# Kernel tuning notes

Measured on AMD Instinct MI355X. Metric: run time of the kernel, lower is better.

Reference implementation:

```python
import jax, jax.numpy as jnp
import numpy as np

B = 16384      # rays
H = 128        # field hidden dim


def setup_inputs() -> dict:
    key = jax.random.key(0)
    ks = jax.random.split(key, 8)
    origins = jax.random.normal(ks[0], (B, 3), dtype=jnp.float32)
    directions = jax.random.normal(ks[1], (B, 3), dtype=jnp.float32)
    directions = directions / jnp.linalg.norm(directions, axis=-1, keepdims=True)
    # Field: simple MLP 3 -> H -> H -> 4 (rgb + sigma)
    W1 = jax.random.normal(ks[2], (3, H), dtype=jnp.float32) * (1.0 / np.sqrt(3.0))
    b1 = jnp.zeros((H,), dtype=jnp.float32)
    W2 = jax.random.normal(ks[3], (H, H), dtype=jnp.float32) * (1.0 / np.sqrt(H))
    b2 = jnp.zeros((H,), dtype=jnp.float32)
    W3 = jax.random.normal(ks[4], (H, 4), dtype=jnp.float32) * (1.0 / np.sqrt(H))
    b3 = jnp.zeros((4,), dtype=jnp.float32)
    return {"origins": origins, "directions": directions,
            "W1": W1, "b1": b1, "W2": W2, "b2": b2, "W3": W3, "b3": b3,
            "near": 2, "far": 6, "num_samples": 64}


def _field(x, W1, b1, W2, b2, W3, b3):
    h = jax.nn.relu(x @ W1 + b1)
    h = jax.nn.relu(h @ W2 + b2)
    return h @ W3 + b3


def reference(origins, directions, W1, b1, W2, b2, W3, b3, near, far, num_samples):
    near = jnp.float32(near)
    far = jnp.float32(far)
    # 1. generate_samples: segment boundaries + midpoints along each ray
    depths = jnp.linspace(near, far, num_samples + 1)            # [S+1]
    midpoints = 0.5 * (depths[:-1] + depths[1:])                 # [S]
    # [B, S, 3] = origin + t * direction
    locs = origins[:, None, :] + midpoints[None, :, None] * directions[:, None, :]
    # 2. evaluate field
    f = _field(locs.reshape(-1, 3), W1, b1, W2, b2, W3, b3)
    f = f.reshape(origins.shape[0], num_samples, 4)
    # NOTE: source overwrites the sigmoid'd colors with raw outputs (faithful)
    colors = f[..., :3]                                          # [B, S, 3]
    sigma = f[..., 3]                                            # [B, S]
    # 3. alpha values
    delta = depths[1:] - depths[:-1]                             # [S]
    alphas = 1.0 - jnp.exp(-sigma * delta[None, :])              # [B, S]
    # 4. alpha compositing (black background)
    ones = jnp.ones_like(alphas[:, :1])
    transmittance = jnp.cumprod(jnp.concatenate([ones, 1.0 - alphas], axis=1), axis=1)[:, :-1]
    weights = alphas * transmittance                             # [B, S]
    radiance = jnp.sum(weights[..., None] * colors, axis=1)      # [B, 3]
    return radiance
```

## Files before the change

### kernel.cpp

```cpp
#include <hip/hip_runtime.h>


typedef _Float16 f16;
typedef __attribute__((ext_vector_type(2))) _Float16 h2v;
typedef __attribute__((ext_vector_type(8))) _Float16 half8;
typedef __attribute__((ext_vector_type(4))) float floatx4;

#define H 128
#define NS 64

static __device__ __forceinline__ h2v pkrtz(float a, float b) {
  return __builtin_bit_cast(h2v, __builtin_amdgcn_cvt_pkrtz(a, b));
}

template <int CTRL, int RM>
static __device__ __forceinline__ float dpp_add(float x) {
  int sh = __builtin_amdgcn_update_dpp(0, __builtin_bit_cast(int, x),
                                       CTRL, RM, 0xf, false);
  return x + __builtin_bit_cast(float, sh);
}

static __device__ __forceinline__ float wave_iscan(float x) {
  x = dpp_add<0x111, 0xf>(x);
  x = dpp_add<0x112, 0xf>(x);
  x = dpp_add<0x114, 0xf>(x);
  x = dpp_add<0x118, 0xf>(x);
  x = dpp_add<0x142, 0xa>(x);
  x = dpp_add<0x143, 0xc>(x);
  return x;
}

__global__ void nerf_setup(const float* __restrict__ W2, const float* __restrict__ W3,
                           f16* __restrict__ wsW2, f16* __restrict__ wsW3) {
  int t = blockIdx.x * blockDim.x + threadIdx.x;
  if (t < 8192) {
    int j2 = t & 3, lane = (t >> 2) & 63, mt = (t >> 8) & 7, ks = t >> 11;
    int l16 = lane & 15;
    int k = ks * 32 + ((lane >> 4) * 8) + 2 * j2;
    int n = 32 * (l16 >> 2) + mt * 4 + (l16 & 3);
    wsW2[2 * t]     = (f16)W2[k * H + n];
    wsW2[2 * t + 1] = (f16)W2[(k + 1) * H + n];
  } else if (t < 9216) {
    int u = t - 8192;
    int j2 = u & 3, lane = (u >> 2) & 63, ks = u >> 8;
    int c = lane & 15;
    int k3 = 32 * (lane >> 4) + ks * 8 + 2 * j2;
    wsW3[2 * u]     = (c < 4) ? (f16)W3[k3 * 4 + c]       : (f16)0.0f;
    wsW3[2 * u + 1] = (c < 4) ? (f16)W3[(k3 + 1) * 4 + c] : (f16)0.0f;
  }
}

__global__ __launch_bounds__(512, 4) void nerf_main(
    const float* __restrict__ origins, const float* __restrict__ dirs,
    const float* __restrict__ W1, const float* __restrict__ b1,
    const float* __restrict__ b2, const float* __restrict__ b3,
    const f16* __restrict__ ws,
    float* __restrict__ out)
{
  __shared__ __align__(16) half8 w_lds[2304];
  __shared__ __align__(16) float b2_lds[H];
  __shared__ __align__(16) f16   popd[8][2][H];
  __shared__ __align__(16) float f_lds[8][64][4];

  const int t = threadIdx.x;
  const int w = t >> 6, lane = t & 63, quad = lane >> 4, l16 = lane & 15;
  const float delta = 4.0f / NS;
  const int ray = blockIdx.x * 8 + w;

  {
    const uint4* src = (const uint4*)ws;
    uint4* dst = (uint4*)w_lds;
    #pragma unroll
    for (int i = 0; i < 4; ++i) dst[t + i * 512] = src[t + i * 512];
    if (t < 256) dst[t + 2048] = src[t + 2048];
    if (t < 32)  ((float4*)b2_lds)[t] = ((const float4*)b2)[t];
  }

  {
    const float o0 = origins[ray*3], o1 = origins[ray*3+1], o2 = origins[ray*3+2];
    const float d0 = dirs[ray*3],    d1 = dirs[ray*3+1],    d2 = dirs[ray*3+2];
    const int k0 = lane * 2;
    const float2 wr0 = *(const float2*)&W1[0*H + k0];
    const float2 wr1 = *(const float2*)&W1[1*H + k0];
    const float2 wr2 = *(const float2*)&W1[2*H + k0];
    const float2 bb  = *(const float2*)&b1[k0];
    float poa = fmaf(o2, wr2.x, fmaf(o1, wr1.x, fmaf(o0, wr0.x, bb.x)));
    float pob = fmaf(o2, wr2.y, fmaf(o1, wr1.y, fmaf(o0, wr0.y, bb.y)));
    float pda = fmaf(d2, wr2.x, fmaf(d1, wr1.x, d0 * wr0.x));
    float pdb = fmaf(d2, wr2.y, fmaf(d1, wr1.y, d0 * wr0.y));
    h2v po2; po2[0] = (f16)poa; po2[1] = (f16)pob;
    h2v pd2; pd2[0] = (f16)pda; pd2[1] = (f16)pdb;
    *(h2v*)&popd[w][0][k0] = po2;
    *(h2v*)&popd[w][1][k0] = pd2;
  }

  half8 hb[4][4];
  {
    const half8 z8 = (half8)(f16)0.0f;
    half8 m8[4];
    #pragma unroll
    for (int tr = 0; tr < 4; ++tr)
      m8[tr] = (half8)(f16)(2.0f + (tr*16 + l16 + 0.5f) * delta);
    #pragma unroll
    for (int ks = 0; ks < 4; ++ks) {
      const half8 po8 = *(const half8*)&popd[w][0][ks*32 + quad*8];
      const half8 pd8 = *(const half8*)&popd[w][1][ks*32 + quad*8];
      #pragma unroll
      for (int tr = 0; tr < 4; ++tr)
        hb[ks][tr] = __builtin_elementwise_max(pd8 * m8[tr] + po8, z8);
    }
  }

  __syncthreads();

  const half8* w2f = w_lds;
  const half8* w3f = w_lds + 2048;
  const h2v z2 = (h2v)(f16)0.0f;

  floatx4 acc3[4];
  {
    const float4 b3v = *(const float4*)&b3[0];
    #pragma unroll
    for (int tr = 0; tr < 4; ++tr) {
      acc3[tr][0] = b3v.x; acc3[tr][1] = b3v.y;
      acc3[tr][2] = b3v.z; acc3[tr][3] = b3v.w;
    }
  }

  #pragma unroll 1
  for (int ks3 = 0; ks3 < 4; ++ks3) {
    const int mt0 = 2 * ks3, mt1 = mt0 + 1;
    const float4 bA = *(const float4*)&b2_lds[quad*32 + mt0*4];
    const float4 bB = *(const float4*)&b2_lds[quad*32 + mt1*4];
    const half8 w3k = w3f[ks3*64 + lane];
    floatx4 accA[4], accB[4];
    #pragma unroll
    for (int tr = 0; tr < 4; ++tr) {
      accA[tr][0] = bA.x; accA[tr][1] = bA.y; accA[tr][2] = bA.z; accA[tr][3] = bA.w;
      accB[tr][0] = bB.x; accB[tr][1] = bB.y; accB[tr][2] = bB.z; accB[tr][3] = bB.w;
    }
    #pragma unroll
    for (int ks2 = 0; ks2 < 4; ++ks2) {
      const half8 wA = w2f[(ks2*8 + mt0)*64 + lane];
      const half8 wB = w2f[(ks2*8 + mt1)*64 + lane];
      #pragma unroll
      for (int tr = 0; tr < 4; ++tr) {
        accA[tr] = __builtin_amdgcn_mfma_f32_16x16x32_f16(wA, hb[ks2][tr], accA[tr], 0, 0, 0);
        accB[tr] = __builtin_amdgcn_mfma_f32_16x16x32_f16(wB, hb[ks2][tr], accB[tr], 0, 0, 0);
      }
    }
    #pragma unroll
    for (int tr = 0; tr < 4; ++tr) {
      h2v c0 = __builtin_elementwise_max(pkrtz(accA[tr][0], accA[tr][1]), z2);
      h2v c1 = __builtin_elementwise_max(pkrtz(accA[tr][2], accA[tr][3]), z2);
      h2v c2 = __builtin_elementwise_max(pkrtz(accB[tr][0], accB[tr][1]), z2);
      h2v c3 = __builtin_elementwise_max(pkrtz(accB[tr][2], accB[tr][3]), z2);
      half8 b = { c0[0], c0[1], c1[0], c1[1], c2[0], c2[1], c3[0], c3[1] };
      acc3[tr] = __builtin_amdgcn_mfma_f32_16x16x32_f16(w3k, b, acc3[tr], 0, 0, 0);
    }
  }

  if (quad == 0) {
    #pragma unroll
    for (int tr = 0; tr < 4; ++tr) {
      float4 fv;
      fv.x = acc3[tr][0]; fv.y = acc3[tr][1];
      fv.z = acc3[tr][2]; fv.w = acc3[tr][3];
      *(float4*)&f_lds[w][tr*16 + l16][0] = fv;
    }
  }

  {
    const float4 fv = *(const float4*)&f_lds[w][lane][0];
    const float sigma = fv.w;
    const float alpha = 1.0f - __expf(-sigma * delta);
    const float S  = wave_iscan(sigma);
    const float T  = __expf(-delta * (S - sigma));
    const float wt = alpha * T;
    const float sr = wave_iscan(wt * fv.x);
    const float sg = wave_iscan(wt * fv.y);
    const float sb = wave_iscan(wt * fv.z);
    if (lane == 63) {
      out[ray*3+0] = sr; out[ray*3+1] = sg; out[ray*3+2] = sb;
    }
  }
}

extern "C" void kernel_launch(void* const* d_in, const int* in_sizes, int n_in,
                              void* d_out, int out_size, void* d_ws, size_t ws_size,
                              hipStream_t stream) {
  const float* origins = (const float*)d_in[0];
  const float* dirs    = (const float*)d_in[1];
  const float* W1      = (const float*)d_in[2];
  const float* b1      = (const float*)d_in[3];
  const float* W2      = (const float*)d_in[4];
  const float* b2      = (const float*)d_in[5];
  const float* W3      = (const float*)d_in[6];
  const float* b3      = (const float*)d_in[7];
  float* out = (float*)d_out;

  f16* wsW2 = (f16*)d_ws;
  f16* wsW3 = wsW2 + 16384;

  nerf_setup<<<36, 256, 0, stream>>>(W2, W3, wsW2, wsW3);
  nerf_main<<<16384 / 8, 512, 0, stream>>>(
      origins, dirs, W1, b1, b2, b3, wsW2, out);
}
```

Measured before the change: 102.6 us.

## Coalesce weight setup via LDS, raise occupancy hint, stagger per-wave layer-2 order

The setup kernel now stages W2 into shared memory with coalesced float4 loads and then writes the permuted fp16 layout, using 9 blocks instead of 36 scattered-read blocks. The main kernel's launch bound moves from 4 to 6 waves-per-EU minimum, which caps register use to allow more resident blocks. The layer-2/3 loop is fully unrolled and each wave starts at a different k-slice ((w+it)&3) so the 8 waves in a block read different LDS regions at the same time. Risks are register spilling under the tighter bound and extra code size from the full unroll.

```diff
diff --git a/kernel.cpp b/kernel.cpp
--- a/kernel.cpp
+++ b/kernel.cpp
@@ -32,25 +32,47 @@
 
 __global__ void nerf_setup(const float* __restrict__ W2, const float* __restrict__ W3,
                            f16* __restrict__ wsW2, f16* __restrict__ wsW3) {
-  int t = blockIdx.x * blockDim.x + threadIdx.x;
-  if (t < 8192) {
-    int j2 = t & 3, lane = (t >> 2) & 63, mt = (t >> 8) & 7, ks = t >> 11;
-    int l16 = lane & 15;
-    int k = ks * 32 + ((lane >> 4) * 8) + 2 * j2;
-    int n = 32 * (l16 >> 2) + mt * 4 + (l16 & 3);
-    wsW2[2 * t]     = (f16)W2[k * H + n];
-    wsW2[2 * t + 1] = (f16)W2[(k + 1) * H + n];
-  } else if (t < 9216) {
-    int u = t - 8192;
-    int j2 = u & 3, lane = (u >> 2) & 63, ks = u >> 8;
-    int c = lane & 15;
-    int k3 = 32 * (lane >> 4) + ks * 8 + 2 * j2;
-    wsW3[2 * u]     = (c < 4) ? (f16)W3[k3 * 4 + c]       : (f16)0.0f;
-    wsW3[2 * u + 1] = (c < 4) ? (f16)W3[(k3 + 1) * 4 + c] : (f16)0.0f;
-  }
-}
-
-__global__ __launch_bounds__(512, 4) void nerf_main(
+  __shared__ __align__(16) f16 w2s[H * H];
+  const int t = threadIdx.x;
+  const int b = blockIdx.x;
+  if (b < 8) {
+    const float4* src = (const float4*)W2;
+    #pragma unroll
+    for (int i = 0; i < 16; ++i) {
+      const float4 v = src[t + i * 256];
+      const int e = (t + i * 256) * 4;
+      h2v p0; p0[0] = (f16)v.x; p0[1] = (f16)v.y;
+      h2v p1; p1[0] = (f16)v.z; p1[1] = (f16)v.w;
+      *(h2v*)&w2s[e]     = p0;
+      *(h2v*)&w2s[e + 2] = p1;
+    }
+    __syncthreads();
+    #pragma unroll
+    for (int j = 0; j < 4; ++j) {
+      const int p = b * 1024 + j * 256 + t;
+      const int j2 = p & 3, lane = (p >> 2) & 63, mt = (p >> 8) & 7, ks = p >> 11;
+      const int l16 = lane & 15;
+      const int k = ks * 32 + ((lane >> 4) * 8) + 2 * j2;
+      const int n = 32 * (l16 >> 2) + mt * 4 + (l16 & 3);
+      h2v pr; pr[0] = w2s[k * H + n]; pr[1] = w2s[(k + 1) * H + n];
+      *(h2v*)&wsW2[2 * p] = pr;
+    }
+  } else {
+    #pragma unroll
+    for (int j = 0; j < 4; ++j) {
+      const int u = j * 256 + t;
+      const int j2 = u & 3, lane = (u >> 2) & 63, ks = u >> 8;
+      const int c = lane & 15;
+      const int k3 = 32 * (lane >> 4) + ks * 8 + 2 * j2;
+      h2v pr;
+      pr[0] = (c < 4) ? (f16)W3[k3 * 4 + c]       : (f16)0.0f;
+      pr[1] = (c < 4) ? (f16)W3[(k3 + 1) * 4 + c] : (f16)0.0f;
+      *(h2v*)&wsW3[2 * u] = pr;
+    }
+  }
+}
+
+__global__ __launch_bounds__(512, 6) void nerf_main(
     const float* __restrict__ origins, const float* __restrict__ dirs,
     const float* __restrict__ W1, const float* __restrict__ b1,
     const float* __restrict__ b2, const float* __restrict__ b3,
@@ -127,11 +149,12 @@
     }
   }
 
-  #pragma unroll 1
-  for (int ks3 = 0; ks3 < 4; ++ks3) {
+  #pragma unroll
+  for (int it = 0; it < 4; ++it) {
+    const int ks3 = (w + it) & 3;
     const int mt0 = 2 * ks3, mt1 = mt0 + 1;
-    const float4 bA = *(const float4*)&b2_lds[quad*32 + mt0*4];
-    const float4 bB = *(const float4*)&b2_lds[quad*32 + mt1*4];
+    const float4 bA = *(const float4*)&b2_lds[quad*32 + ks3*8];
+    const float4 bB = *(const float4*)&b2_lds[quad*32 + ks3*8 + 4];
     const half8 w3k = w3f[ks3*64 + lane];
     floatx4 accA[4], accB[4];
     #pragma unroll
@@ -202,7 +225,7 @@
   f16* wsW2 = (f16*)d_ws;
   f16* wsW3 = wsW2 + 16384;
 
-  nerf_setup<<<36, 256, 0, stream>>>(W2, W3, wsW2, wsW3);
+  nerf_setup<<<9, 256, 0, stream>>>(W2, W3, wsW2, wsW3);
   nerf_main<<<16384 / 8, 512, 0, stream>>>(
       origins, dirs, W1, b1, b2, b3, wsW2, out);
 }
```

Measured after the change: 278.1 us. 2.71x slower.
